# Kernel optimization log

Hardware: AMD Instinct MI355X
Metric: run time of the kernel (lower is better)

## Reference

```python
import jax, jax.numpy as jnp
import numpy as np

B, T, H, V = 32, 16, 768, 32000
EPS = 1e-5


def _conv(x, w, stride, pad):
    return jax.lax.conv_general_dilated(
        x, w, (stride, stride), [(pad, pad), (pad, pad)],
        dimension_numbers=('NCHW', 'OIHW', 'NCHW'))


def _bn(x, g, b, m, v):
    inv = g / jnp.sqrt(v + EPS)
    return x * inv[None, :, None, None] + (b - m * inv)[None, :, None, None]


def setup_inputs() -> dict:
    key = jax.random.key(0)
    ks = iter(jax.random.split(key, 48))

    def rn(shape, s=0.02):
        return s * jax.random.normal(next(ks), shape, jnp.float32)

    def bn_params(c):
        g = 1.0 + 0.1 * jax.random.normal(next(ks), (c,), jnp.float32)
        b = 0.1 * jax.random.normal(next(ks), (c,), jnp.float32)
        m = 0.1 * jax.random.normal(next(ks), (c,), jnp.float32)
        v = jax.random.uniform(next(ks), (c,), jnp.float32, 0.5, 1.5)
        return g, b, m, v

    inp = {}
    inp['images'] = jax.random.normal(next(ks), (B, 3, 224, 224), jnp.float32)
    inp['captions'] = jax.random.randint(next(ks), (B, T), 0, V)

    inp['conv1_w'] = rn((64, 3, 7, 7))
    inp['bn1_g'], inp['bn1_b'], inp['bn1_m'], inp['bn1_v'] = bn_params(64)
    inp['conv2_w'] = rn((128, 64, 3, 3))
    inp['bn2_g'], inp['bn2_b'], inp['bn2_m'], inp['bn2_v'] = bn_params(128)
    inp['conv3_w'] = rn((256, 128, 3, 3))
    inp['bn3_g'], inp['bn3_b'], inp['bn3_m'], inp['bn3_v'] = bn_params(256)
    inp['conv4_w'] = rn((H, 256, 3, 3))
    inp['bn4_g'], inp['bn4_b'], inp['bn4_m'], inp['bn4_v'] = bn_params(H)

    emb = rn((V, H), 1.0)
    inp['emb_table'] = emb.at[0].set(0.0)  # padding_idx=0 row is zero
    inp['attn_w'] = rn((H, H))             # attn_proj (no bias)
    inp['w_ih'] = rn((4 * H, 2 * H))       # LSTM input weights (i,f,g,o)
    inp['w_hh'] = rn((4 * H, H))
    inp['b_ih'] = rn((4 * H,))
    inp['b_hh'] = rn((4 * H,))
    inp['fc_w'] = rn((V, H))
    inp['fc_b'] = rn((V,))
    return inp


def _forward(images, captions, conv1_w, bn1_g, bn1_b, bn1_m, bn1_v,
             conv2_w, bn2_g, bn2_b, bn2_m, bn2_v,
             conv3_w, bn3_g, bn3_b, bn3_m, bn3_v,
             conv4_w, bn4_g, bn4_b, bn4_m, bn4_v,
             emb_table, attn_w, w_ih, w_hh, b_ih, b_hh, fc_w, fc_b):
    # ---- ResNetEncoder ----
    x = jax.nn.relu(_bn(_conv(images, conv1_w, 2, 3), bn1_g, bn1_b, bn1_m, bn1_v))
    x = jax.lax.reduce_window(x, -jnp.inf, jax.lax.max, (1, 1, 3, 3), (1, 1, 2, 2),
                              ((0, 0), (0, 0), (1, 1), (1, 1)))
    x = jax.nn.relu(_bn(_conv(x, conv2_w, 1, 1), bn2_g, bn2_b, bn2_m, bn2_v))
    x = jax.nn.relu(_bn(_conv(x, conv3_w, 2, 1), bn3_g, bn3_b, bn3_m, bn3_v))
    x = jax.nn.relu(_bn(_conv(x, conv4_w, 1, 1), bn4_g, bn4_b, bn4_m, bn4_v))
    b, c, hh, ww = x.shape
    memory = x.reshape(b, c, hh * ww).transpose(0, 2, 1)[:, :196, :]  # [B,196,H]

    # ---- LSTMAttnDecoder ----
    emb = emb_table[captions]  # [B,T,H]
    h0 = jnp.zeros((b, H), jnp.float32)
    c0 = jnp.zeros((b, H), jnp.float32)

    def step(carry, e_t):
        h, cst = carry
        q = h @ attn_w.T                                    # [B,H]
        scores = jnp.einsum('bh,bmh->bm', q, memory)        # [B,196]
        ctx = jnp.einsum('bm,bmh->bh', jax.nn.softmax(scores, axis=-1), memory)
        xin = jnp.concatenate([e_t, ctx], axis=-1)          # [B,2H]
        gates = xin @ w_ih.T + b_ih + h @ w_hh.T + b_hh     # [B,4H]
        i, f, g, o = jnp.split(gates, 4, axis=-1)
        c_new = jax.nn.sigmoid(f) * cst + jax.nn.sigmoid(i) * jnp.tanh(g)
        h_new = jax.nn.sigmoid(o) * jnp.tanh(c_new)
        logits = h_new @ fc_w.T + fc_b                      # [B,V]
        return (h_new, c_new), logits

    (hT, cT), logits = jax.lax.scan(step, (h0, c0), emb.transpose(1, 0, 2))
    logits = logits.transpose(1, 0, 2)  # [B,T,V]
    return logits, (hT[None], cT[None])


def reference(images, captions, conv1_w, bn1_g, bn1_b, bn1_m, bn1_v,
              conv2_w, bn2_g, bn2_b, bn2_m, bn2_v,
              conv3_w, bn3_g, bn3_b, bn3_m, bn3_v,
              conv4_w, bn4_g, bn4_b, bn4_m, bn4_v,
              emb_table, attn_w, w_ih, w_hh, b_ih, b_hh, fc_w, fc_b):
    return _forward(images, captions, conv1_w, bn1_g, bn1_b, bn1_m, bn1_v,
                    conv2_w, bn2_g, bn2_b, bn2_m, bn2_v,
                    conv3_w, bn3_g, bn3_b, bn3_m, bn3_v,
                    conv4_w, bn4_g, bn4_b, bn4_m, bn4_v,
                    emb_table, attn_w, w_ih, w_hh, b_ih, b_hh, fc_w, fc_b)
```

## Files before the change

kernel.cpp:

```cpp
#include <hip/hip_runtime.h>
#include <math.h>

#define NB 32
#define NT 16
#define NH 768
#define NV 32000

typedef short bf16x8 __attribute__((ext_vector_type(8)));
typedef float floatx4 __attribute__((ext_vector_type(4)));
typedef unsigned short ushort_t;

__device__ __forceinline__ float bf2f(unsigned short h) {
    unsigned u = ((unsigned)h) << 16;
    return __builtin_bit_cast(float, u);
}
__device__ __forceinline__ unsigned short f2bf(float f) {
    unsigned u = __builtin_bit_cast(unsigned, f);
    u += 0x7fffu + ((u >> 16) & 1u);
    return (unsigned short)(u >> 16);
}
__device__ __forceinline__ float sigmoidf_(float x) { return 1.f / (1.f + expf(-x)); }

__device__ __forceinline__ bf16x8 cvt8(float4 a, float4 b) {
    bf16x8 t;
    t[0] = (short)f2bf(a.x); t[1] = (short)f2bf(a.y);
    t[2] = (short)f2bf(a.z); t[3] = (short)f2bf(a.w);
    t[4] = (short)f2bf(b.x); t[5] = (short)f2bf(b.y);
    t[6] = (short)f2bf(b.z); t[7] = (short)f2bf(b.w);
    return t;
}

__global__ __launch_bounds__(256) void bn_prep4(
    const float* __restrict__ g1, const float* __restrict__ b1, const float* __restrict__ m1, const float* __restrict__ v1,
    const float* __restrict__ g2, const float* __restrict__ b2, const float* __restrict__ m2, const float* __restrict__ v2,
    const float* __restrict__ g3, const float* __restrict__ b3, const float* __restrict__ m3, const float* __restrict__ v3,
    const float* __restrict__ g4, const float* __restrict__ b4, const float* __restrict__ m4, const float* __restrict__ v4,
    float* __restrict__ s1, float* __restrict__ o1, float* __restrict__ s2, float* __restrict__ o2,
    float* __restrict__ s3, float* __restrict__ o3, float* __restrict__ s4, float* __restrict__ o4) {
    int i = blockIdx.x * 256 + threadIdx.x;
    const float *g, *b, *m, *v;
    float *s, *o;
    int c;
    if (i < 64)        { g = g1; b = b1; m = m1; v = v1; s = s1; o = o1; c = i; }
    else if (i < 192)  { g = g2; b = b2; m = m2; v = v2; s = s2; o = o2; c = i - 64; }
    else if (i < 448)  { g = g3; b = b3; m = m3; v = v3; s = s3; o = o3; c = i - 192; }
    else if (i < 1216) { g = g4; b = b4; m = m4; v = v4; s = s4; o = o4; c = i - 448; }
    else return;
    float inv = g[c] * rsqrtf(v[c] + 1e-5f);
    s[c] = inv;
    o[c] = b[c] - m[c] * inv;
}

__global__ __launch_bounds__(256) void zfill(unsigned long long* __restrict__ p, long long n) {
    long long i = (long long)blockIdx.x * 256 + threadIdx.x;
    if (i < n) p[i] = 0ULL;
}

__global__ __launch_bounds__(256) void cvt_packW_conv(const float* __restrict__ w, ushort_t* __restrict__ dst,
                                                      int CIN, int total) {
    int idx = blockIdx.x * 256 + threadIdx.x;
    if (idx >= total) return;
    int e = idx & 7, lane = (idx >> 3) & 63, j = (idx >> 9) & 3;
    int r = idx >> 11;
    int KQ = CIN >> 5;
    int kq = r % KQ; r /= KQ;
    int tap = r % 9; int nt = r / 9;
    int co = nt * 64 + j * 16 + (lane & 15);
    int ci = kq * 32 + (lane >> 4) * 8 + e;
    dst[idx] = f2bf(w[((size_t)co * CIN + ci) * 9 + tap]);
}

__global__ __launch_bounds__(256) void cvt_wcombP(const float* __restrict__ w_ih, const float* __restrict__ w_hh,
                                                  ushort_t* __restrict__ dst) {
    int idx = blockIdx.x * 256 + threadIdx.x;
    if (idx >= 3072 * 1536) return;
    int e = idx & 7, lane = (idx >> 3) & 63;
    int t = idx >> 9;
    int kq = t % 48, gg = t / 48;
    int g = gg & 3, bx = gg >> 2;
    int j = g * 768 + bx * 16 + (lane & 15);
    int k = kq * 32 + (lane >> 4) * 8 + e;
    float v = (k < NH) ? w_ih[(size_t)j * (2 * NH) + NH + k] : w_hh[(size_t)j * NH + (k - NH)];
    dst[idx] = f2bf(v);
}

__global__ __launch_bounds__(256) void cvt_wattnTP(const float* __restrict__ w, ushort_t* __restrict__ dst) {
    int idx = blockIdx.x * 256 + threadIdx.x;
    if (idx >= 768 * 768) return;
    int e = idx & 7, lane = (idx >> 3) & 63, j = (idx >> 9) & 3;
    int t = idx >> 11;
    int kq = t % 24, nt = t / 24;
    int n = nt * 64 + 16 * j + (lane & 15);
    int k = kq * 32 + (lane >> 4) * 8 + e;
    dst[idx] = f2bf(w[(size_t)k * 768 + n]);
}

__global__ __launch_bounds__(256) void cvt_pad(const float* __restrict__ src, ushort_t* __restrict__ dst) {
    int idx = blockIdx.x * 256 + threadIdx.x;
    if (idx >= 64 * 160) return;
    int co = idx / 160, k = idx % 160;
    dst[idx] = (k < 147) ? f2bf(src[co * 147 + k]) : (ushort_t)0;
}

__global__ __launch_bounds__(256) void im2col1(const float* __restrict__ img, ushort_t* __restrict__ A) {
    int idx = blockIdx.x * 256 + threadIdx.x;
    const int total = 121856 * 160;
    if (idx >= total) return;
    int k = idx % 160;
    int m = idx / 160;
    ushort_t v = 0;
    if (k < 147) {
        int b = m / 3808;
        int rm = m % 3808;
        int y = rm / 112, x = rm % 112;
        int ci = k / 49;
        int r = k % 49;
        int ky = r / 7, kx = r % 7;
        int iy = 2 * y - 3 + ky;
        int ix = 2 * x - 3 + kx;
        if ((unsigned)iy < 224u && (unsigned)ix < 224u)
            v = f2bf(img[((size_t)(b * 3 + ci) * 224 + iy) * 224 + ix]);
    }
    A[idx] = v;
}

__global__ __launch_bounds__(256) void conv1_gemm(
    const ushort_t* __restrict__ A, const ushort_t* __restrict__ Bw,
    const float* __restrict__ scale, const float* __restrict__ bias,
    ushort_t* __restrict__ out) {
    int lane = threadIdx.x & 63, w = threadIdx.x >> 6;
    int m0 = (blockIdx.x * 4 + w) * 64;
    int lr = lane & 15, kl = (lane >> 4) * 8;
    floatx4 acc[4][4];
    #pragma unroll
    for (int i = 0; i < 4; ++i)
        #pragma unroll
        for (int j = 0; j < 4; ++j) acc[i][j] = 0.f;
    #pragma unroll
    for (int k0 = 0; k0 < 160; k0 += 32) {
        bf16x8 a[4], bb[4];
        #pragma unroll
        for (int i = 0; i < 4; ++i) a[i] = *(const bf16x8*)(A + (size_t)(m0 + 16 * i + lr) * 160 + kl + k0);
        #pragma unroll
        for (int j = 0; j < 4; ++j) bb[j] = *(const bf16x8*)(Bw + (size_t)(16 * j + lr) * 160 + kl + k0);
        #pragma unroll
        for (int i = 0; i < 4; ++i)
            #pragma unroll
            for (int j = 0; j < 4; ++j)
                acc[i][j] = __builtin_amdgcn_mfma_f32_16x16x32_bf16(a[i], bb[j], acc[i][j], 0, 0, 0);
    }
    #pragma unroll
    for (int i = 0; i < 4; ++i) {
        #pragma unroll
        for (int r = 0; r < 4; ++r) {
            int m = m0 + 16 * i + (lane >> 4) * 4 + r;
            int b = m / 3808;
            int rm = m % 3808;
            int y = rm / 112, x = rm % 112;
            #pragma unroll
            for (int j = 0; j < 4; ++j) {
                int n = 16 * j + lr;
                float v = fmaxf(acc[i][j][r] * scale[n] + bias[n], 0.f);
                out[((size_t)(b * 34 + y) * 112 + x) * 64 + n] = f2bf(v);
            }
        }
    }
}

__global__ __launch_bounds__(256) void pool_kernel(const ushort_t* __restrict__ in,
                                                   ushort_t* __restrict__ hal2) {
    int idx = blockIdx.x * 256 + threadIdx.x;
    const int total = 32 * 17 * 56 * 8;
    if (idx >= total) return;
    int c8 = idx & 7;
    int rest = idx >> 3;
    int x = rest % 56; rest /= 56;
    int y = rest % 17; int b = rest / 17;
    float mx[8];
    #pragma unroll
    for (int j = 0; j < 8; ++j) mx[j] = -INFINITY;
    for (int dy = -1; dy <= 1; ++dy) {
        int iy = 2 * y + dy;
        if ((unsigned)iy >= 34u) continue;
        for (int dx = -1; dx <= 1; ++dx) {
            int ix = 2 * x + dx;
            if ((unsigned)ix >= 112u) continue;
            bf16x8 v = *(const bf16x8*)(in + (((size_t)(b * 34 + iy)) * 112 + ix) * 64 + c8 * 8);
            #pragma unroll
            for (int j = 0; j < 8; ++j) mx[j] = fmaxf(mx[j], bf2f((unsigned short)v[j]));
        }
    }
    bf16x8 o;
    #pragma unroll
    for (int j = 0; j < 8; ++j) o[j] = (short)f2bf(mx[j]);
    *(bf16x8*)(hal2 + (((size_t)(b * 19 + y + 1)) * 58 + (x + 1)) * 64 + c8 * 8) = o;
}

template <int CIN, int HH, int WH, int STRIDE, int HOUT, int WOUT, int COUT, int MEMOUT, int OH, int OW>
__global__ __launch_bounds__(64) void conv_mfma(
    const ushort_t* __restrict__ in, const ushort_t* __restrict__ wtP,
    const float* __restrict__ scale, const float* __restrict__ bias,
    ushort_t* __restrict__ out) {
    int lane = threadIdx.x;
    int mt = blockIdx.x, nt = blockIdx.y;
    int lr = lane & 15, kl = (lane >> 4) * 8;
    int rowoff[4];
    #pragma unroll
    for (int i = 0; i < 4; ++i) {
        int m = mt * 64 + 16 * i + lr;
        int b = m / (HOUT * WOUT);
        int rm = m % (HOUT * WOUT);
        int y = rm / WOUT, x = rm % WOUT;
        rowoff[i] = ((b * HH + y * STRIDE) * WH + x * STRIDE) * CIN + kl;
    }
    floatx4 acc[4][4];
    #pragma unroll
    for (int i = 0; i < 4; ++i)
        #pragma unroll
        for (int j = 0; j < 4; ++j) acc[i][j] = 0.f;

    #pragma unroll
    for (int ky = 0; ky < 3; ++ky) {
        #pragma unroll
        for (int kx = 0; kx < 3; ++kx) {
            int ioff = (ky * WH + kx) * CIN;
            int t = ky * 3 + kx;
            #pragma unroll
            for (int k0 = 0; k0 < CIN; k0 += 32) {
                bf16x8 a[4], bb[4];
                #pragma unroll
                for (int i = 0; i < 4; ++i)
                    a[i] = *(const bf16x8*)(in + rowoff[i] + ioff + k0);
                #pragma unroll
                for (int j = 0; j < 4; ++j)
                    bb[j] = *(const bf16x8*)(wtP + ((((size_t)(nt * 9 + t) * (CIN / 32) + (k0 >> 5)) * 4 + j) * 64 + lane) * 8);
                #pragma unroll
                for (int i = 0; i < 4; ++i)
                    #pragma unroll
                    for (int j = 0; j < 4; ++j)
                        acc[i][j] = __builtin_amdgcn_mfma_f32_16x16x32_bf16(a[i], bb[j], acc[i][j], 0, 0, 0);
            }
        }
    }
    #pragma unroll
    for (int i = 0; i < 4; ++i) {
        #pragma unroll
        for (int r = 0; r < 4; ++r) {
            int m = mt * 64 + 16 * i + (lane >> 4) * 4 + r;
            int b = m / (HOUT * WOUT);
            int rm = m % (HOUT * WOUT);
            int y = rm / WOUT, x = rm % WOUT;
            #pragma unroll
            for (int j = 0; j < 4; ++j) {
                int n = nt * 64 + 16 * j + lr;
                float v = fmaxf(acc[i][j][r] * scale[n] + bias[n], 0.f);
                ushort_t hv = f2bf(v);
                if (MEMOUT) {
                    out[(size_t)m * COUT + n] = hv;
                } else {
                    out[((size_t)(b * OH + y + 1) * OW + (x + 1)) * COUT + n] = hv;
                }
            }
        }
    }
}

__global__ __launch_bounds__(64) void kmat_gemm(
    const ushort_t* __restrict__ memv, const ushort_t* __restrict__ Bp,
    ushort_t* __restrict__ KT) {
    int lane = threadIdx.x;
    int mt = blockIdx.x, nt = blockIdx.y;
    int lr = lane & 15, kl = (lane >> 4) * 8;
    floatx4 acc[4][4];
    #pragma unroll
    for (int i = 0; i < 4; ++i)
        #pragma unroll
        for (int j = 0; j < 4; ++j) acc[i][j] = 0.f;
    for (int kq = 0; kq < 24; ++kq) {
        bf16x8 a[4], bb[4];
        #pragma unroll
        for (int i = 0; i < 4; ++i)
            a[i] = *(const bf16x8*)(memv + (size_t)(mt * 64 + 16 * i + lr) * 768 + kq * 32 + kl);
        #pragma unroll
        for (int j = 0; j < 4; ++j)
            bb[j] = *(const bf16x8*)(Bp + (((size_t)(nt * 24 + kq) * 4 + j) * 64 + lane) * 8);
        #pragma unroll
        for (int i = 0; i < 4; ++i)
            #pragma unroll
            for (int j = 0; j < 4; ++j)
                acc[i][j] = __builtin_amdgcn_mfma_f32_16x16x32_bf16(a[i], bb[j], acc[i][j], 0, 0, 0);
    }
    #pragma unroll
    for (int i = 0; i < 4; ++i) {
        #pragma unroll
        for (int r = 0; r < 4; ++r) {
            int mg = mt * 64 + 16 * i + (lane >> 4) * 4 + r;
            int b = mg / 196, m = mg % 196;
            #pragma unroll
            for (int j = 0; j < 4; ++j) {
                int n = nt * 64 + 16 * j + lr;
                KT[(((size_t)b * 96 + (n >> 3)) * 196 + m) * 8 + (n & 7)] = f2bf(acc[i][j][r]);
            }
        }
    }
}

__global__ __launch_bounds__(256) void gather_embP(const int* __restrict__ caps,
                                                   const float* __restrict__ table,
                                                   ushort_t* __restrict__ dst) {
    int idx = blockIdx.x * 256 + threadIdx.x;
    if (idx >= 512 * 768) return;
    int e = idx & 7, lane = (idx >> 3) & 63, i = (idx >> 9) & 3;
    int t2 = idx >> 11;
    int kq = t2 % 24, mt = t2 / 24;
    int r = mt * 64 + i * 16 + (lane & 15);
    int k = kq * 32 + (lane >> 4) * 8 + e;
    int t = r >> 5, b = r & 31;
    dst[idx] = f2bf(table[(size_t)caps[b * NT + t] * NH + k]);
}

template <int REMAP>
__global__ __launch_bounds__(256) void gemm_pipe(
    const ushort_t* __restrict__ Ap, const float* __restrict__ B,
    const float* __restrict__ bias1, const float* __restrict__ bias2,
    float* __restrict__ C, int ldb, int N) {
    __shared__ ushort_t bl[2][2048];
    int tid = threadIdx.x;
    int lane = tid & 63, w = tid >> 6;
    int nt = blockIdx.x;
    int r = tid >> 2, c0 = (tid & 3) * 8;
    const float* bsrc = B + (size_t)(nt * 64 + r) * ldb + c0;
    int slotoff = (((r >> 4) * 64 + ((r & 15) | ((tid & 3) << 4))) * 8);
    ushort_t* slot0 = &bl[0][0] + slotoff;
    ushort_t* slot1 = &bl[1][0] + slotoff;
    floatx4 acc[2][4][4];
    #pragma unroll
    for (int h = 0; h < 2; ++h)
        #pragma unroll
        for (int i = 0; i < 4; ++i)
            #pragma unroll
            for (int j = 0; j < 4; ++j) acc[h][i][j] = 0.f;

    float4 p0a = *(const float4*)(bsrc),      p0b = *(const float4*)(bsrc + 4);
    float4 fa0 = *(const float4*)(bsrc + 32), fa1 = *(const float4*)(bsrc + 36);
    float4 fb0 = *(const float4*)(bsrc + 64), fb1 = *(const float4*)(bsrc + 68);
    *(bf16x8*)slot0 = cvt8(p0a, p0b);

    for (int j = 0; j < 24; ++j) {
        __syncthreads();
        if (j < 23) {
            *(bf16x8*)((j & 1) ? slot0 : slot1) = cvt8(fa0, fa1);
            fa0 = fb0; fa1 = fb1;
        }
        if (j < 21) {
            const float* p = bsrc + (size_t)(j + 3) * 32;
            fb0 = *(const float4*)p;
            fb1 = *(const float4*)(p + 4);
        }
        const ushort_t* rb = &bl[j & 1][0];
        bf16x8 bb[4];
        #pragma unroll
        for (int j4 = 0; j4 < 4; ++j4) bb[j4] = *(const bf16x8*)(rb + (j4 * 64 + lane) * 8);
        #pragma unroll
        for (int h = 0; h < 2; ++h) {
            int mt = w + h * 4;
            bf16x8 a[4];
            #pragma unroll
            for (int i = 0; i < 4; ++i)
                a[i] = *(const bf16x8*)(Ap + ((((size_t)mt * 24 + j) * 4 + i) * 64 + lane) * 8);
            #pragma unroll
            for (int i = 0; i < 4; ++i)
                #pragma unroll
                for (int j4 = 0; j4 < 4; ++j4)
                    acc[h][i][j4] = __builtin_amdgcn_mfma_f32_16x16x32_bf16(a[i], bb[j4], acc[h][i][j4], 0, 0, 0);
        }
    }
    int lr = lane & 15;
    #pragma unroll
    for (int h = 0; h < 2; ++h) {
        int mt = w + h * 4;
        #pragma unroll
        for (int i = 0; i < 4; ++i) {
            #pragma unroll
            for (int rr = 0; rr < 4; ++rr) {
                int m = mt * 64 + 16 * i + (lane >> 4) * 4 + rr;
                #pragma unroll
                for (int j4 = 0; j4 < 4; ++j4) {
                    int n = nt * 64 + 16 * j4 + lr;
                    float vv = acc[h][i][j4][rr];
                    if (bias1) vv += bias1[n];
                    if (bias2) vv += bias2[n];
                    if (REMAP) {
                        int t = m >> 5, b = m & 31;
                        C[(size_t)((b << 4) + t) * NV + n] = vv;
                    } else {
                        C[(size_t)m * N + n] = vv;
                    }
                }
            }
        }
    }
}

__global__ __launch_bounds__(768) void attn2(
    ushort_t* __restrict__ xin, const ushort_t* __restrict__ KT,
    const ushort_t* __restrict__ mem) {
    __shared__ float hq[NH];
    __shared__ float sl[196];
    __shared__ float red[16];
    int b = blockIdx.x, tid = threadIdx.x;
    hq[tid] = bf2f(xin[(size_t)b * 1536 + NH + tid]);
    __syncthreads();
    if (tid < 392) {
        int m = tid >> 1, half = tid & 1;
        const ushort_t* basep = KT + (((size_t)b * 96 + half * 48) * 196 + m) * 8;
        float acc = 0.f;
        #pragma unroll 4
        for (int k8 = 0; k8 < 48; ++k8) {
            bf16x8 v = *(const bf16x8*)(basep + (size_t)k8 * 196 * 8);
            const float* qp = hq + (half * 48 + k8) * 8;
            #pragma unroll
            for (int j = 0; j < 8; ++j)
                acc = fmaf(bf2f((unsigned short)v[j]), qp[j], acc);
        }
        acc += __shfl_xor(acc, 1);
        if (!half) sl[m] = acc;
    }
    __syncthreads();
    float sc = (tid < 196) ? sl[tid] : -INFINITY;
    float v = sc;
    #pragma unroll
    for (int off = 32; off; off >>= 1) v = fmaxf(v, __shfl_down(v, off));
    if ((tid & 63) == 0) red[tid >> 6] = v;
    __syncthreads();
    if (tid == 0) {
        float m = red[0];
        for (int i = 1; i < 12; ++i) m = fmaxf(m, red[i]);
        red[12] = m;
    }
    __syncthreads();
    float mx = red[12];
    float e = (tid < 196) ? expf(sc - mx) : 0.f;
    __syncthreads();
    v = e;
    #pragma unroll
    for (int off = 32; off; off >>= 1) v += __shfl_down(v, off);
    if ((tid & 63) == 0) red[tid >> 6] = v;
    __syncthreads();
    if (tid == 0) {
        float s = red[0];
        for (int i = 1; i < 12; ++i) s += red[i];
        red[12] = 1.f / s;
    }
    __syncthreads();
    if (tid < 196) sl[tid] = e * red[12];
    __syncthreads();
    {
        float acc = 0.f;
        const ushort_t* mb = mem + (size_t)b * 196 * NH + tid;
        #pragma unroll 4
        for (int m = 0; m < 196; ++m) acc = fmaf(sl[m], bf2f(mb[(size_t)m * NH]), acc);
        xin[(size_t)b * 1536 + tid] = f2bf(acc);
    }
}

__global__ __launch_bounds__(256) void step_fused(
    const ushort_t* __restrict__ xin_r, const ushort_t* __restrict__ wcombP,
    const float* __restrict__ eg_t,
    float* __restrict__ cbuf, float* __restrict__ hbuf,
    ushort_t* __restrict__ xin_w, ushort_t* __restrict__ hallP, int tstep) {
    __shared__ float pbuf[4][64][33];
    int lane = threadIdx.x & 63, w = threadIdx.x >> 6;
    int bx = blockIdx.x;
    int lr = lane & 15, kl = (lane >> 4) * 8;
    floatx4 acc[2][4];
    #pragma unroll
    for (int i = 0; i < 2; ++i)
        #pragma unroll
        for (int g = 0; g < 4; ++g) acc[i][g] = 0.f;
    for (int kq = 0; kq < 12; ++kq) {
        int k = w * 384 + kq * 32;
        bf16x8 a[2], bb[4];
        #pragma unroll
        for (int i = 0; i < 2; ++i)
            a[i] = *(const bf16x8*)(xin_r + (size_t)(16 * i + lr) * 1536 + k + kl);
        #pragma unroll
        for (int g = 0; g < 4; ++g)
            bb[g] = *(const bf16x8*)(wcombP + (((size_t)(bx * 4 + g) * 48 + (w * 12 + kq)) * 64 + lane) * 8);
        #pragma unroll
        for (int i = 0; i < 2; ++i)
            #pragma unroll
            for (int g = 0; g < 4; ++g)
                acc[i][g] = __builtin_amdgcn_mfma_f32_16x16x32_bf16(a[i], bb[g], acc[i][g], 0, 0, 0);
    }
    #pragma unroll
    for (int i = 0; i < 2; ++i)
        #pragma unroll
        for (int g = 0; g < 4; ++g)
            #pragma unroll
            for (int r = 0; r < 4; ++r) {
                int m = 16 * i + (lane >> 4) * 4 + r;
                pbuf[w][g * 16 + lr][m] = acc[i][g][r];
            }
    __syncthreads();
    int tid = threadIdx.x;
    #pragma unroll
    for (int o = 0; o < 2; ++o) {
        int pid = tid * 2 + o;
        int m = pid & 31, c = pid >> 5;
        int kcol = bx * 16 + c;
        float gi = 0.f, gf = 0.f, gg = 0.f, go = 0.f;
        #pragma unroll
        for (int ww = 0; ww < 4; ++ww) {
            gi += pbuf[ww][c][m];
            gf += pbuf[ww][16 + c][m];
            gg += pbuf[ww][32 + c][m];
            go += pbuf[ww][48 + c][m];
        }
        const float* eg = eg_t + (size_t)m * 3072;
        gi += eg[kcol];
        gf += eg[768 + kcol];
        gg += eg[1536 + kcol];
        go += eg[2304 + kcol];
        float cst = cbuf[m * 768 + kcol];
        float cn = sigmoidf_(gf) * cst + sigmoidf_(gi) * tanhf(gg);
        float hn = sigmoidf_(go) * tanhf(cn);
        cbuf[m * 768 + kcol] = cn;
        hbuf[m * 768 + kcol] = hn;
        ushort_t hb = f2bf(hn);
        xin_w[(size_t)m * 1536 + NH + kcol] = hb;
        int rrow = tstep * 32 + m;
        int mtp = rrow >> 6, ip = (rrow >> 4) & 3, lrp = rrow & 15;
        int kqp = kcol >> 5, hip = (kcol >> 3) & 3, ep = kcol & 7;
        hallP[((((size_t)mtp * 24 + kqp) * 4 + ip) * 64 + (lrp | (hip << 4))) * 8 + ep] = hb;
    }
}

__global__ __launch_bounds__(256) void zero_state(float* __restrict__ h, float* __restrict__ c,
                                                  ushort_t* __restrict__ xin) {
    int i = blockIdx.x * 256 + threadIdx.x;
    if (i < NB * 1536) xin[i] = 0;
    if (i < NB * NH) { h[i] = 0.f; c[i] = 0.f; }
}

__global__ __launch_bounds__(256) void copy_hc(const float* __restrict__ h, const float* __restrict__ c,
                                               float* __restrict__ out) {
    int i = blockIdx.x * 256 + threadIdx.x;
    if (i < NB * NH) {
        out[(size_t)NB * NT * NV + i] = h[i];
        out[(size_t)NB * NT * NV + NB * NH + i] = c[i];
    }
}

extern "C" void kernel_launch(void* const* d_in, const int* in_sizes, int n_in,
                              void* d_out, int out_size, void* d_ws, size_t ws_size,
                              hipStream_t stream) {
    const float* images   = (const float*)d_in[0];
    const int*   captions = (const int*)d_in[1];
    const float* conv1_w  = (const float*)d_in[2];
    const float* bn1_g = (const float*)d_in[3], *bn1_b = (const float*)d_in[4];
    const float* bn1_m = (const float*)d_in[5], *bn1_v = (const float*)d_in[6];
    const float* conv2_w  = (const float*)d_in[7];
    const float* bn2_g = (const float*)d_in[8], *bn2_b = (const float*)d_in[9];
    const float* bn2_m = (const float*)d_in[10], *bn2_v = (const float*)d_in[11];
    const float* conv3_w  = (const float*)d_in[12];
    const float* bn3_g = (const float*)d_in[13], *bn3_b = (const float*)d_in[14];
    const float* bn3_m = (const float*)d_in[15], *bn3_v = (const float*)d_in[16];
    const float* conv4_w  = (const float*)d_in[17];
    const float* bn4_g = (const float*)d_in[18], *bn4_b = (const float*)d_in[19];
    const float* bn4_m = (const float*)d_in[20], *bn4_v = (const float*)d_in[21];
    const float* emb_table = (const float*)d_in[22];
    const float* attn_w   = (const float*)d_in[23];
    const float* w_ih     = (const float*)d_in[24];
    const float* w_hh     = (const float*)d_in[25];
    const float* b_ih     = (const float*)d_in[26];
    const float* b_hh     = (const float*)d_in[27];
    const float* fc_w     = (const float*)d_in[28];
    const float* fc_b     = (const float*)d_in[29];
    float* out = (float*)d_out;

    char* base = (char*)d_ws;
    size_t off = 0;
    auto alloc = [&](size_t bytes) { char* p = base + off; off += (bytes + 255) & ~(size_t)255; return p; };
    float* s1 = (float*)alloc(64 * 4);   float* bb1 = (float*)alloc(64 * 4);
    float* s2 = (float*)alloc(128 * 4);  float* bb2 = (float*)alloc(128 * 4);
    float* s3 = (float*)alloc(256 * 4);  float* bb3 = (float*)alloc(256 * 4);
    float* s4 = (float*)alloc(768 * 4);  float* bb4 = (float*)alloc(768 * 4);
    ushort_t* c1out = (ushort_t*)alloc((size_t)32 * 34 * 112 * 64 * 2);
    size_t halo_start = off;
    ushort_t* hal2 = (ushort_t*)alloc((size_t)32 * 19 * 58 * 64 * 2);
    ushort_t* hal3 = (ushort_t*)alloc((size_t)32 * 18 * 58 * 128 * 2);
    ushort_t* hal4 = (ushort_t*)alloc((size_t)32 * 10 * 30 * 256 * 2);
    size_t halo_bytes = off - halo_start;
    ushort_t* memv = (ushort_t*)alloc((size_t)32 * 196 * 768 * 2);
    ushort_t* KT   = (ushort_t*)alloc((size_t)32 * 96 * 196 * 8 * 2);
    ushort_t* wb1 = (ushort_t*)alloc((size_t)64 * 160 * 2);
    ushort_t* wb2 = (ushort_t*)alloc((size_t)128 * 9 * 64 * 2);
    ushort_t* wb3 = (ushort_t*)alloc((size_t)256 * 9 * 128 * 2);
    ushort_t* wb4 = (ushort_t*)alloc((size_t)768 * 9 * 256 * 2);
    ushort_t* wattnTP = (ushort_t*)alloc((size_t)768 * 768 * 2);
    ushort_t* wcombP = (ushort_t*)alloc((size_t)3072 * 1536 * 2);
    ushort_t* e512P = (ushort_t*)alloc((size_t)512 * 768 * 2);
    float* eg   = (float*)alloc((size_t)512 * 3072 * 4);
    ushort_t* HallP = (ushort_t*)alloc((size_t)512 * 768 * 2);
    float* hbuf = (float*)alloc(NB * NH * 4);
    float* cbuf = (float*)alloc(NB * NH * 4);
    ushort_t* xinA = (ushort_t*)alloc((size_t)NB * 1536 * 2);
    ushort_t* xinB = (ushort_t*)alloc((size_t)NB * 1536 * 2);
    ushort_t* imcol = (ushort_t*)alloc((size_t)121856 * 160 * 2);

    bn_prep4<<<5, 256, 0, stream>>>(bn1_g, bn1_b, bn1_m, bn1_v,
                                    bn2_g, bn2_b, bn2_m, bn2_v,
                                    bn3_g, bn3_b, bn3_m, bn3_v,
                                    bn4_g, bn4_b, bn4_m, bn4_v,
                                    s1, bb1, s2, bb2, s3, bb3, s4, bb4);
    cvt_pad<<<(64 * 160 + 255) / 256, 256, 0, stream>>>(conv1_w, wb1);
    cvt_packW_conv<<<(128 * 9 * 64 + 255) / 256, 256, 0, stream>>>(conv2_w, wb2, 64, 128 * 9 * 64);
    cvt_packW_conv<<<(256 * 9 * 128 + 255) / 256, 256, 0, stream>>>(conv3_w, wb3, 128, 256 * 9 * 128);
    cvt_packW_conv<<<(768 * 9 * 256 + 255) / 256, 256, 0, stream>>>(conv4_w, wb4, 256, 768 * 9 * 256);
    cvt_wattnTP<<<(768 * 768 + 255) / 256, 256, 0, stream>>>(attn_w, wattnTP);
    cvt_wcombP<<<(3072 * 1536 + 255) / 256, 256, 0, stream>>>(w_ih, w_hh, wcombP);
    {
        long long n8 = (long long)(halo_bytes / 8);
        zfill<<<(unsigned)((n8 + 255) / 256), 256, 0, stream>>>((unsigned long long*)hal2, n8);
    }

    im2col1<<<(121856 * 160 + 255) / 256, 256, 0, stream>>>(images, imcol);
    conv1_gemm<<<476, 256, 0, stream>>>(imcol, wb1, s1, bb1, c1out);
    pool_kernel<<<(32 * 17 * 56 * 8 + 255) / 256, 256, 0, stream>>>(c1out, hal2);
    conv_mfma<64, 19, 58, 1, 16, 56, 128, 0, 18, 58>
        <<<dim3(448, 2), 64, 0, stream>>>(hal2, wb2, s2, bb2, hal3);
    conv_mfma<128, 18, 58, 2, 8, 28, 256, 0, 10, 30>
        <<<dim3(112, 4), 64, 0, stream>>>(hal3, wb3, s3, bb3, hal4);
    conv_mfma<256, 10, 30, 1, 7, 28, 768, 1, 1, 1>
        <<<dim3(98, 12), 64, 0, stream>>>(hal4, wb4, s4, bb4, memv);

    kmat_gemm<<<dim3(98, 12), 64, 0, stream>>>(memv, wattnTP, KT);

    gather_embP<<<(512 * 768) / 256, 256, 0, stream>>>(captions, emb_table, e512P);
    gemm_pipe<0><<<48, 256, 0, stream>>>(e512P, w_ih, b_ih, b_hh, eg, 2 * NH, 3072);
    zero_state<<<(NB * 1536 + 255) / 256, 256, 0, stream>>>(hbuf, cbuf, xinA);

    ushort_t* xcur = xinA;
    ushort_t* xnxt = xinB;
    for (int t = 0; t < NT; ++t) {
        attn2<<<NB, NH, 0, stream>>>(xcur, KT, memv);
        step_fused<<<48, 256, 0, stream>>>(
            xcur, wcombP, eg + (size_t)t * NB * 3072, cbuf, hbuf, xnxt, HallP, t);
        ushort_t* tmp = xcur; xcur = xnxt; xnxt = tmp;
    }

    gemm_pipe<1><<<500, 256, 0, stream>>>(HallP, fc_w, fc_b, nullptr, out, NH, NV);

    copy_hc<<<(NB * NH + 255) / 256, 256, 0, stream>>>(hbuf, cbuf, out);
}
```

Before: 923.3 us.

## Stage four K-chunks per barrier with swizzled LDS in projection GEMMs

The B-operand staging in the GEMM used for the input-gate and vocab projections changes from a double buffer that advances one 32-wide K chunk per barrier to a batch of four chunks per stage. Each stage now covers 128 K values with two barriers, and the next group's global loads are issued before the MFMA work. An XOR swizzle on the LDS byte offsets is added to reduce bank conflicts on the staged bf16 tiles. The aim is fewer barriers per K step and more memory-level parallelism, at the cost of more registers for the prefetched data and a larger LDS footprint, which could lower occupancy.

```diff
diff --git a/kernel.cpp b/kernel.cpp
--- a/kernel.cpp
+++ b/kernel.cpp
@@ -319,20 +319,19 @@
     dst[idx] = f2bf(table[(size_t)caps[b * NT + t] * NH + k]);
 }
 
+#define LSWZ(byteoff) ((byteoff) ^ ((((byteoff) >> 8) & 3) << 4))
 template <int REMAP>
-__global__ __launch_bounds__(256) void gemm_pipe(
+__global__ __launch_bounds__(256) void gemm_pipe4(
     const ushort_t* __restrict__ Ap, const float* __restrict__ B,
     const float* __restrict__ bias1, const float* __restrict__ bias2,
     float* __restrict__ C, int ldb, int N) {
-    __shared__ ushort_t bl[2][2048];
+    __shared__ char bl[4][4096];
     int tid = threadIdx.x;
     int lane = tid & 63, w = tid >> 6;
     int nt = blockIdx.x;
     int r = tid >> 2, c0 = (tid & 3) * 8;
     const float* bsrc = B + (size_t)(nt * 64 + r) * ldb + c0;
-    int slotoff = (((r >> 4) * 64 + ((r & 15) | ((tid & 3) << 4))) * 8);
-    ushort_t* slot0 = &bl[0][0] + slotoff;
-    ushort_t* slot1 = &bl[1][0] + slotoff;
+    int sbyte = LSWZ((((r >> 4) * 64 + ((r & 15) | ((tid & 3) << 4))) * 16));
     floatx4 acc[2][4][4];
     #pragma unroll
     for (int h = 0; h < 2; ++h)
@@ -341,38 +340,45 @@
             #pragma unroll
             for (int j = 0; j < 4; ++j) acc[h][i][j] = 0.f;
 
-    float4 p0a = *(const float4*)(bsrc),      p0b = *(const float4*)(bsrc + 4);
-    float4 fa0 = *(const float4*)(bsrc + 32), fa1 = *(const float4*)(bsrc + 36);
-    float4 fb0 = *(const float4*)(bsrc + 64), fb1 = *(const float4*)(bsrc + 68);
-    *(bf16x8*)slot0 = cvt8(p0a, p0b);
-
-    for (int j = 0; j < 24; ++j) {
+    float4 g0a = *(const float4*)(bsrc),       g0b = *(const float4*)(bsrc + 4);
+    float4 g1a = *(const float4*)(bsrc + 32),  g1b = *(const float4*)(bsrc + 36);
+    float4 g2a = *(const float4*)(bsrc + 64),  g2b = *(const float4*)(bsrc + 68);
+    float4 g3a = *(const float4*)(bsrc + 96),  g3b = *(const float4*)(bsrc + 100);
+
+    for (int g = 0; g < 6; ++g) {
         __syncthreads();
-        if (j < 23) {
-            *(bf16x8*)((j & 1) ? slot0 : slot1) = cvt8(fa0, fa1);
-            fa0 = fb0; fa1 = fb1;
-        }
-        if (j < 21) {
-            const float* p = bsrc + (size_t)(j + 3) * 32;
-            fb0 = *(const float4*)p;
-            fb1 = *(const float4*)(p + 4);
-        }
-        const ushort_t* rb = &bl[j & 1][0];
-        bf16x8 bb[4];
-        #pragma unroll
-        for (int j4 = 0; j4 < 4; ++j4) bb[j4] = *(const bf16x8*)(rb + (j4 * 64 + lane) * 8);
-        #pragma unroll
-        for (int h = 0; h < 2; ++h) {
-            int mt = w + h * 4;
-            bf16x8 a[4];
-            #pragma unroll
-            for (int i = 0; i < 4; ++i)
-                a[i] = *(const bf16x8*)(Ap + ((((size_t)mt * 24 + j) * 4 + i) * 64 + lane) * 8);
-            #pragma unroll
-            for (int i = 0; i < 4; ++i)
+        *(bf16x8*)(&bl[0][0] + sbyte) = cvt8(g0a, g0b);
+        *(bf16x8*)(&bl[1][0] + sbyte) = cvt8(g1a, g1b);
+        *(bf16x8*)(&bl[2][0] + sbyte) = cvt8(g2a, g2b);
+        *(bf16x8*)(&bl[3][0] + sbyte) = cvt8(g3a, g3b);
+        if (g < 5) {
+            const float* p = bsrc + (size_t)(g + 1) * 128;
+            g0a = *(const float4*)(p);       g0b = *(const float4*)(p + 4);
+            g1a = *(const float4*)(p + 32);  g1b = *(const float4*)(p + 36);
+            g2a = *(const float4*)(p + 64);  g2b = *(const float4*)(p + 68);
+            g3a = *(const float4*)(p + 96);  g3b = *(const float4*)(p + 100);
+        }
+        __syncthreads();
+        #pragma unroll
+        for (int cc = 0; cc < 4; ++cc) {
+            int kq = g * 4 + cc;
+            bf16x8 bb[4];
+            #pragma unroll
+            for (int j4 = 0; j4 < 4; ++j4)
+                bb[j4] = *(const bf16x8*)(&bl[cc][0] + LSWZ(((j4 * 64 + lane) * 16)));
+            #pragma unroll
+            for (int h = 0; h < 2; ++h) {
+                int mt = w + h * 4;
+                bf16x8 a[4];
                 #pragma unroll
-                for (int j4 = 0; j4 < 4; ++j4)
-                    acc[h][i][j4] = __builtin_amdgcn_mfma_f32_16x16x32_bf16(a[i], bb[j4], acc[h][i][j4], 0, 0, 0);
+                for (int i = 0; i < 4; ++i)
+                    a[i] = *(const bf16x8*)(Ap + ((((size_t)mt * 24 + kq) * 4 + i) * 64 + lane) * 8);
+                #pragma unroll
+                for (int i = 0; i < 4; ++i)
+                    #pragma unroll
+                    for (int j4 = 0; j4 < 4; ++j4)
+                        acc[h][i][j4] = __builtin_amdgcn_mfma_f32_16x16x32_bf16(a[i], bb[j4], acc[h][i][j4], 0, 0, 0);
+            }
         }
     }
     int lr = lane & 15;
@@ -638,7 +644,7 @@
     kmat_gemm<<<dim3(98, 12), 64, 0, stream>>>(memv, wattnTP, KT);
 
     gather_embP<<<(512 * 768) / 256, 256, 0, stream>>>(captions, emb_table, e512P);
-    gemm_pipe<0><<<48, 256, 0, stream>>>(e512P, w_ih, b_ih, b_hh, eg, 2 * NH, 3072);
+    gemm_pipe4<0><<<48, 256, 0, stream>>>(e512P, w_ih, b_ih, b_hh, eg, 2 * NH, 3072);
     zero_state<<<(NB * 1536 + 255) / 256, 256, 0, stream>>>(hbuf, cbuf, xinA);
 
     ushort_t* xcur = xinA;
@@ -650,7 +656,7 @@
         ushort_t* tmp = xcur; xcur = xnxt; xnxt = tmp;
     }
 
-    gemm_pipe<1><<<500, 256, 0, stream>>>(HallP, fc_w, fc_b, nullptr, out, NH, NV);
+    gemm_pipe4<1><<<500, 256, 0, stream>>>(HallP, fc_w, fc_b, nullptr, out, NH, NV);
 
     copy_hc<<<(NB * NH + 255) / 256, 256, 0, stream>>>(hbuf, cbuf, out);
 }
```

Result: no change. 937.2 us (+1.5%).

## Pre-convert FC and w_ih weights to bf16 and split GEMMs over M halves

Applied to the files above, without the earlier changes.

Adds a row-wise fp32-to-bf16 conversion pass for fc_w and the input half of w_ih, so the projection GEMMs load bf16 B tiles straight into padded LDS instead of converting fp32 on the fly. The GEMM is rewritten to use 64-wide K chunks with a padded LDS layout, and the M dimension is split across two blocks in y, which doubles the grid and halves per-block accumulators. The fc_w bf16 copy reuses the im2col buffer after conv1. The cost is an extra conversion kernel that reads the whole 32000x768 fc_w each call, plus B tiles loaded twice across the two M halves.

```diff
diff --git a/kernel.cpp b/kernel.cpp
--- a/kernel.cpp
+++ b/kernel.cpp
@@ -56,6 +56,16 @@
     if (i < n) p[i] = 0ULL;
 }
 
+__global__ __launch_bounds__(256) void cvt_b16rows(const float* __restrict__ src, ushort_t* __restrict__ dst,
+                                                   int cols8, int ldsrc, int total8) {
+    int i = blockIdx.x * 256 + threadIdx.x;
+    if (i >= total8) return;
+    int r = i / cols8, g = i % cols8;
+    const float4* s = (const float4*)(src + (size_t)r * ldsrc + g * 8);
+    float4 a = s[0], b = s[1];
+    *(bf16x8*)(dst + (size_t)i * 8) = cvt8(a, b);
+}
+
 __global__ __launch_bounds__(256) void cvt_packW_conv(const float* __restrict__ w, ushort_t* __restrict__ dst,
                                                       int CIN, int total) {
     int idx = blockIdx.x * 256 + threadIdx.x;
@@ -320,82 +330,71 @@
 }
 
 template <int REMAP>
-__global__ __launch_bounds__(256) void gemm_pipe(
-    const ushort_t* __restrict__ Ap, const float* __restrict__ B,
+__global__ __launch_bounds__(256, 4) void gemm_ldsb(
+    const ushort_t* __restrict__ Ap, const ushort_t* __restrict__ Bb,
     const float* __restrict__ bias1, const float* __restrict__ bias2,
-    float* __restrict__ C, int ldb, int N) {
-    __shared__ ushort_t bl[2][2048];
+    float* __restrict__ C, int N) {
+    __shared__ ushort_t bt[2][64 * 72];
     int tid = threadIdx.x;
     int lane = tid & 63, w = tid >> 6;
-    int nt = blockIdx.x;
-    int r = tid >> 2, c0 = (tid & 3) * 8;
-    const float* bsrc = B + (size_t)(nt * 64 + r) * ldb + c0;
-    int slotoff = (((r >> 4) * 64 + ((r & 15) | ((tid & 3) << 4))) * 8);
-    ushort_t* slot0 = &bl[0][0] + slotoff;
-    ushort_t* slot1 = &bl[1][0] + slotoff;
-    floatx4 acc[2][4][4];
-    #pragma unroll
-    for (int h = 0; h < 2; ++h)
-        #pragma unroll
-        for (int i = 0; i < 4; ++i)
-            #pragma unroll
-            for (int j = 0; j < 4; ++j) acc[h][i][j] = 0.f;
-
-    float4 p0a = *(const float4*)(bsrc),      p0b = *(const float4*)(bsrc + 4);
-    float4 fa0 = *(const float4*)(bsrc + 32), fa1 = *(const float4*)(bsrc + 36);
-    float4 fb0 = *(const float4*)(bsrc + 64), fb1 = *(const float4*)(bsrc + 68);
-    *(bf16x8*)slot0 = cvt8(p0a, p0b);
-
-    for (int j = 0; j < 24; ++j) {
+    int nt = blockIdx.x, mh = blockIdx.y;
+    int n0 = nt * 64;
+    int mt = mh * 4 + w;
+    int lr = lane & 15, hi = lane >> 4;
+    int srow = tid >> 2, sc = tid & 3;
+    const ushort_t* gsrc = Bb + (size_t)(n0 + srow) * 768 + sc * 8;
+    int woff = srow * 72 + sc * 8;
+    floatx4 acc[4][4];
+    #pragma unroll
+    for (int i = 0; i < 4; ++i)
+        #pragma unroll
+        for (int j = 0; j < 4; ++j) acc[i][j] = 0.f;
+    bf16x8 s0 = *(const bf16x8*)(gsrc);
+    bf16x8 s1 = *(const bf16x8*)(gsrc + 32);
+    for (int kc = 0; kc < 12; ++kc) {
+        ushort_t* bufw = &bt[kc & 1][0];
+        *(bf16x8*)(bufw + woff) = s0;
+        *(bf16x8*)(bufw + woff + 32) = s1;
+        if (kc < 11) {
+            const ushort_t* p = gsrc + (size_t)(kc + 1) * 64;
+            s0 = *(const bf16x8*)(p);
+            s1 = *(const bf16x8*)(p + 32);
+        }
         __syncthreads();
-        if (j < 23) {
-            *(bf16x8*)((j & 1) ? slot0 : slot1) = cvt8(fa0, fa1);
-            fa0 = fb0; fa1 = fb1;
-        }
-        if (j < 21) {
-            const float* p = bsrc + (size_t)(j + 3) * 32;
-            fb0 = *(const float4*)p;
-            fb1 = *(const float4*)(p + 4);
-        }
-        const ushort_t* rb = &bl[j & 1][0];
-        bf16x8 bb[4];
-        #pragma unroll
-        for (int j4 = 0; j4 < 4; ++j4) bb[j4] = *(const bf16x8*)(rb + (j4 * 64 + lane) * 8);
-        #pragma unroll
-        for (int h = 0; h < 2; ++h) {
-            int mt = w + h * 4;
-            bf16x8 a[4];
+        const ushort_t* bufr = &bt[kc & 1][0];
+        #pragma unroll
+        for (int kk = 0; kk < 2; ++kk) {
+            int kq = kc * 2 + kk;
+            bf16x8 bfr[4], a[4];
+            #pragma unroll
+            for (int j = 0; j < 4; ++j)
+                bfr[j] = *(const bf16x8*)(bufr + (j * 16 + lr) * 72 + kk * 32 + hi * 8);
             #pragma unroll
             for (int i = 0; i < 4; ++i)
-                a[i] = *(const bf16x8*)(Ap + ((((size_t)mt * 24 + j) * 4 + i) * 64 + lane) * 8);
+                a[i] = *(const bf16x8*)(Ap + ((((size_t)mt * 24 + kq) * 4 + i) * 64 + lane) * 8);
             #pragma unroll
             for (int i = 0; i < 4; ++i)
                 #pragma unroll
-                for (int j4 = 0; j4 < 4; ++j4)
-                    acc[h][i][j4] = __builtin_amdgcn_mfma_f32_16x16x32_bf16(a[i], bb[j4], acc[h][i][j4], 0, 0, 0);
-        }
-    }
-    int lr = lane & 15;
-    #pragma unroll
-    for (int h = 0; h < 2; ++h) {
-        int mt = w + h * 4;
-        #pragma unroll
-        for (int i = 0; i < 4; ++i) {
-            #pragma unroll
-            for (int rr = 0; rr < 4; ++rr) {
-                int m = mt * 64 + 16 * i + (lane >> 4) * 4 + rr;
-                #pragma unroll
-                for (int j4 = 0; j4 < 4; ++j4) {
-                    int n = nt * 64 + 16 * j4 + lr;
-                    float vv = acc[h][i][j4][rr];
-                    if (bias1) vv += bias1[n];
-                    if (bias2) vv += bias2[n];
-                    if (REMAP) {
-                        int t = m >> 5, b = m & 31;
-                        C[(size_t)((b << 4) + t) * NV + n] = vv;
-                    } else {
-                        C[(size_t)m * N + n] = vv;
-                    }
+                for (int j = 0; j < 4; ++j)
+                    acc[i][j] = __builtin_amdgcn_mfma_f32_16x16x32_bf16(a[i], bfr[j], acc[i][j], 0, 0, 0);
+        }
+    }
+    #pragma unroll
+    for (int i = 0; i < 4; ++i) {
+        #pragma unroll
+        for (int rr = 0; rr < 4; ++rr) {
+            int m = mt * 64 + 16 * i + hi * 4 + rr;
+            #pragma unroll
+            for (int j = 0; j < 4; ++j) {
+                int n = n0 + 16 * j + lr;
+                float vv = acc[i][j][rr];
+                if (bias1) vv += bias1[n];
+                if (bias2) vv += bias2[n];
+                if (REMAP) {
+                    int t = m >> 5, b = m & 31;
+                    C[(size_t)((b << 4) + t) * NV + n] = vv;
+                } else {
+                    C[(size_t)m * N + n] = vv;
                 }
             }
         }
@@ -600,6 +599,7 @@
     ushort_t* wb4 = (ushort_t*)alloc((size_t)768 * 9 * 256 * 2);
     ushort_t* wattnTP = (ushort_t*)alloc((size_t)768 * 768 * 2);
     ushort_t* wcombP = (ushort_t*)alloc((size_t)3072 * 1536 * 2);
+    ushort_t* wihL = (ushort_t*)alloc((size_t)3072 * 768 * 2);
     ushort_t* e512P = (ushort_t*)alloc((size_t)512 * 768 * 2);
     float* eg   = (float*)alloc((size_t)512 * 3072 * 4);
     ushort_t* HallP = (ushort_t*)alloc((size_t)512 * 768 * 2);
@@ -607,7 +607,9 @@
     float* cbuf = (float*)alloc(NB * NH * 4);
     ushort_t* xinA = (ushort_t*)alloc((size_t)NB * 1536 * 2);
     ushort_t* xinB = (ushort_t*)alloc((size_t)NB * 1536 * 2);
-    ushort_t* imcol = (ushort_t*)alloc((size_t)121856 * 160 * 2);
+    char* ubig = alloc((size_t)NV * NH * 2);
+    ushort_t* imcol = (ushort_t*)ubig;
+    ushort_t* fcwb  = (ushort_t*)ubig;
 
     bn_prep4<<<5, 256, 0, stream>>>(bn1_g, bn1_b, bn1_m, bn1_v,
                                     bn2_g, bn2_b, bn2_m, bn2_v,
@@ -620,6 +622,7 @@
     cvt_packW_conv<<<(768 * 9 * 256 + 255) / 256, 256, 0, stream>>>(conv4_w, wb4, 256, 768 * 9 * 256);
     cvt_wattnTP<<<(768 * 768 + 255) / 256, 256, 0, stream>>>(attn_w, wattnTP);
     cvt_wcombP<<<(3072 * 1536 + 255) / 256, 256, 0, stream>>>(w_ih, w_hh, wcombP);
+    cvt_b16rows<<<(3072 * 96 + 255) / 256, 256, 0, stream>>>(w_ih, wihL, 96, 1536, 3072 * 96);
     {
         long long n8 = (long long)(halo_bytes / 8);
         zfill<<<(unsigned)((n8 + 255) / 256), 256, 0, stream>>>((unsigned long long*)hal2, n8);
@@ -627,6 +630,7 @@
 
     im2col1<<<(121856 * 160 + 255) / 256, 256, 0, stream>>>(images, imcol);
     conv1_gemm<<<476, 256, 0, stream>>>(imcol, wb1, s1, bb1, c1out);
+    cvt_b16rows<<<(NV * 96 + 255) / 256, 256, 0, stream>>>(fc_w, fcwb, 96, 768, NV * 96);
     pool_kernel<<<(32 * 17 * 56 * 8 + 255) / 256, 256, 0, stream>>>(c1out, hal2);
     conv_mfma<64, 19, 58, 1, 16, 56, 128, 0, 18, 58>
         <<<dim3(448, 2), 64, 0, stream>>>(hal2, wb2, s2, bb2, hal3);
@@ -638,7 +642,7 @@
     kmat_gemm<<<dim3(98, 12), 64, 0, stream>>>(memv, wattnTP, KT);
 
     gather_embP<<<(512 * 768) / 256, 256, 0, stream>>>(captions, emb_table, e512P);
-    gemm_pipe<0><<<48, 256, 0, stream>>>(e512P, w_ih, b_ih, b_hh, eg, 2 * NH, 3072);
+    gemm_ldsb<0><<<dim3(48, 2), 256, 0, stream>>>(e512P, wihL, b_ih, b_hh, eg, 3072);
     zero_state<<<(NB * 1536 + 255) / 256, 256, 0, stream>>>(hbuf, cbuf, xinA);
 
     ushort_t* xcur = xinA;
@@ -650,7 +654,7 @@
         ushort_t* tmp = xcur; xcur = xnxt; xnxt = tmp;
     }
 
-    gemm_pipe<1><<<500, 256, 0, stream>>>(HallP, fc_w, fc_b, nullptr, out, NH, NV);
+    gemm_ldsb<1><<<dim3(500, 2), 256, 0, stream>>>(HallP, fcwb, fc_b, nullptr, out, NV);
 
     copy_hc<<<(NB * NH + 255) / 256, 256, 0, stream>>>(hbuf, cbuf, out);
 }
```

Measured after the change: 904.4 us. 2.0% less time.
